# Performance work log

Hardware: AMD Instinct MI355X
Metric: run time of the kernel (lower is better)

The kernel has to match this reference:

```python
import jax, jax.numpy as jnp
import numpy as np

BS, NA, NT, ED, AD, NC = 64, 900, 600, 256, 11, 10
CONF_DECAY = 0.6


def _topk_gather(conf, k, *xs):
    # conf: [bs, N] -> top-k values + gather rows of each x: [bs, N, d] -> [bs, k, d]
    vals, idx = jax.lax.top_k(conf, k)
    outs = [jnp.take_along_axis(x, idx[:, :, None], axis=1) for x in xs]
    return vals, outs


def setup_inputs() -> dict:
    key = jax.random.key(0)
    ks = jax.random.split(key, 7)
    return {
        "instance_feature": jax.random.normal(ks[0], (BS, NA, ED), jnp.float32),
        "anchor": jax.random.normal(ks[1], (BS, NA, AD), jnp.float32),
        "confidence": jax.random.normal(ks[2], (BS, NA, NC), jnp.float32),
        "cached_feature": jax.random.normal(ks[3], (BS, NT, ED), jnp.float32),
        "cached_anchor": jax.random.normal(ks[4], (BS, NT, AD), jnp.float32),
        "prev_confidence": jax.random.uniform(ks[5], (BS, NT), jnp.float32),
        "mask": jax.random.bernoulli(ks[6], 0.8, (BS,)),
    }


def reference(instance_feature, anchor, confidence, cached_feature, cached_anchor, prev_confidence, mask):
    # ---- InstanceBank.update ----
    N = NA - NT  # number of fresh instances kept alongside the temporal cache
    conf_max = confidence.max(axis=-1)  # [bs, NA]
    _, (sel_f, sel_a) = _topk_gather(conf_max, N, instance_feature, anchor)
    sel_f = jnp.concatenate([cached_feature, sel_f], axis=1)  # [bs, NA, ED]
    sel_a = jnp.concatenate([cached_anchor, sel_a], axis=1)   # [bs, NA, AD]
    m = mask[:, None, None]
    feat = jnp.where(m, sel_f, instance_feature)
    anc = jnp.where(m, sel_a, anchor)

    # ---- InstanceBank.cache (detached path) ----
    conf_c = jax.nn.sigmoid(jax.lax.stop_gradient(conf_max))
    conf_c = conf_c.at[:, :NT].set(jnp.maximum(prev_confidence * CONF_DECAY, conf_c[:, :NT]))
    new_conf, (cf, ca) = _topk_gather(
        conf_c, NT, jax.lax.stop_gradient(feat), jax.lax.stop_gradient(anc)
    )

    merged = jnp.concatenate([feat, anc], axis=-1)  # [bs, NA, ED+AD]
    return merged, new_conf, cf, ca
```

## Files before the change

kernel.cpp:

```cpp
#include <hip/hip_runtime.h>

#define BS   64
#define NA   900
#define NT   600
#define NSEL 300
#define ED   256
#define AD   11
#define NC   10
#define SORTN 1024
#define CACHED_FLAG 0x40000000

#define OFF_MERGED  0
#define OFF_NEWCONF (BS * NA * (ED + AD))
#define OFF_CF      (OFF_NEWCONF + BS * NT)
#define OFF_CA      (OFF_CF + BS * NT * ED)

__device__ __forceinline__ unsigned int fkey(float x) {
    unsigned int u = __float_as_uint(x);
    return (u & 0x80000000u) ? ~u : (u | 0x80000000u);
}

__device__ __forceinline__ unsigned long long shfl_xor64(unsigned long long v, int m) {
    return (unsigned long long)__shfl_xor((long long)v, m, 64);
}

__device__ __forceinline__ void sort1024(unsigned long long& key, int i,
                                         unsigned long long* lds) {
    for (int k = 2; k <= SORTN; k <<= 1) {
        for (int j = k >> 1; j > 0; j >>= 1) {
            unsigned long long partner;
            if (j >= 64) {
                __syncthreads();
                lds[i] = key;
                __syncthreads();
                partner = lds[i ^ j];
            } else {
                partner = shfl_xor64(key, j);
            }
            const bool up      = ((i & k) == 0);
            const bool lower   = ((i & j) == 0);
            const bool keepmin = (lower == up);
            const bool pgt     = (key > partner);
            key = (keepmin == pgt) ? partner : key;
        }
    }
}

__global__ __launch_bounds__(1024) void topk_kernel(
    const float* __restrict__ confidence,
    const float* __restrict__ prev_conf,
    const int*   __restrict__ mask,
    float*       __restrict__ new_conf_out,
    int*         __restrict__ src_map,
    int*         __restrict__ pos2)
{
    __shared__ unsigned long long keys[SORTN];
    __shared__ float cc_s[NA];

    const int b = blockIdx.x;
    const int i = threadIdx.x;

    float cmax = 0.0f;
    if (i < NA) {
        const float* cp = confidence + ((size_t)b * NA + i) * NC;
        float m = cp[0];
        #pragma unroll
        for (int k = 1; k < NC; k++) m = fmaxf(m, cp[k]);
        cmax = m;
    }

    unsigned long long key = (i < NA)
        ? ((((unsigned long long)(~fkey(cmax))) << 32) | (unsigned int)i)
        : 0xFFFFFFFFFFFFFFFFull;
    sort1024(key, i, keys);

    __syncthreads();
    int* rank = (int*)keys;
    rank[i] = (int)(key & 0xFFFFFFFFull);
    __syncthreads();

    const int mk = mask[b];
    if (i < NA) {
        int s;
        if (mk) {
            s = (i < NT) ? (i | CACHED_FLAG) : rank[i - NT];
        } else {
            s = i;
        }
        src_map[(size_t)b * NA + i] = s;
    }

    float c = 0.0f;
    if (i < NA) {
        double d = 1.0 / (1.0 + exp(-(double)cmax));
        c = (float)d;
        if (i < NT) c = fmaxf(prev_conf[(size_t)b * NT + i] * 0.6f, c);
        cc_s[i] = c;
    }
    __syncthreads();

    key = (i < NA)
        ? ((((unsigned long long)(~fkey(c))) << 32) | (unsigned int)i)
        : 0xFFFFFFFFFFFFFFFFull;
    sort1024(key, i, keys);

    if (i < NT) {
        int r = (int)(key & 0xFFFFFFFFull);
        new_conf_out[(size_t)b * NT + i] = cc_s[r];
        pos2[(size_t)b * NA + r] = i;
    } else if (i < NA) {
        int r = (int)(key & 0xFFFFFFFFull);
        pos2[(size_t)b * NA + r] = -1;
    }
}

__global__ __launch_bounds__(256) void gather_kernel(
    const float* __restrict__ inst_f,
    const float* __restrict__ anchor,
    const float* __restrict__ cached_f,
    const float* __restrict__ cached_a,
    const int*   __restrict__ src_map,
    const int*   __restrict__ pos2,
    float*       __restrict__ out)
{
    const int wave = threadIdx.x >> 6;
    const int lane = threadIdx.x & 63;
    const int gr   = blockIdx.x * 4 + wave;
    if (gr >= BS * NA) return;

    const int b = gr / NA;
    const int t = gr - b * NA;

    const int s = src_map[(size_t)b * NA + t];
    const int p = pos2[(size_t)b * NA + t];

    const float* fsrc;
    const float* asrc;
    if (s & CACHED_FLAG) {
        const int r = s & 0xFFFF;
        fsrc = cached_f + ((size_t)b * NT + r) * ED;
        asrc = cached_a + ((size_t)b * NT + r) * AD;
    } else {
        fsrc = inst_f + ((size_t)b * NA + s) * ED;
        asrc = anchor + ((size_t)b * NA + s) * AD;
    }

    const float4 v = ((const float4*)fsrc)[lane];
    float av = 0.0f;
    if (lane < AD) av = asrc[lane];

    float* orow = out + OFF_MERGED + ((size_t)b * NA + t) * (ED + AD);
    orow[4 * lane + 0] = v.x;
    orow[4 * lane + 1] = v.y;
    orow[4 * lane + 2] = v.z;
    orow[4 * lane + 3] = v.w;
    if (lane < AD) orow[ED + lane] = av;

    if (p >= 0) {
        float4* crow = (float4*)(out + OFF_CF + ((size_t)b * NT + p) * ED);
        crow[lane] = v;
        if (lane < AD) out[OFF_CA + ((size_t)b * NT + p) * AD + lane] = av;
    }
}

extern "C" void kernel_launch(void* const* d_in, const int* in_sizes, int n_in,
                              void* d_out, int out_size, void* d_ws, size_t ws_size,
                              hipStream_t stream) {
    const float* inst_f = (const float*)d_in[0];
    const float* anchor = (const float*)d_in[1];
    const float* conf   = (const float*)d_in[2];
    const float* cach_f = (const float*)d_in[3];
    const float* cach_a = (const float*)d_in[4];
    const float* prevc  = (const float*)d_in[5];
    const int*   mask   = (const int*)d_in[6];
    float* out = (float*)d_out;

    int* src_map = (int*)d_ws;
    int* pos2    = src_map + BS * NA;

    topk_kernel<<<BS, 1024, 0, stream>>>(conf, prevc, mask,
                                         out + OFF_NEWCONF, src_map, pos2);

    const int nrows = BS * NA;
    gather_kernel<<<(nrows + 3) / 4, 256, 0, stream>>>(
        inst_f, anchor, cach_f, cach_a, src_map, pos2, out);
}
```

Measured before the change: 208.4 us.

## Split the two top-k sorts into separate blocks and use nontemporal gather accesses

The top-k kernel now launches two blocks per batch. One block sorts the raw max-confidence values to build the source map and skips the sort entirely when the mask is off. The other block sorts the sigmoid/decayed confidences for the cache outputs. This doubles block-level parallelism for the serial bitonic sorts, at the cost of computing the per-row confidence max twice. The gather kernel also switches its loads and stores to nontemporal builtins to avoid polluting the cache on the streaming copy.

New measurement: 190.3 us (median of 2 runs). 8.7% less time.

```diff
diff --git a/kernel.cpp b/kernel.cpp
--- a/kernel.cpp
+++ b/kernel.cpp
@@ -14,6 +14,8 @@
 #define OFF_NEWCONF (BS * NA * (ED + AD))
 #define OFF_CF      (OFF_NEWCONF + BS * NT)
 #define OFF_CA      (OFF_CF + BS * NT * ED)
+
+typedef float f32x4 __attribute__((ext_vector_type(4)));
 
 __device__ __forceinline__ unsigned int fkey(float x) {
     unsigned int u = __float_as_uint(x);
@@ -46,6 +48,15 @@
     }
 }
 
+__device__ __forceinline__ float conf_max_row(const float* __restrict__ confidence,
+                                              int b, int i) {
+    const float* cp = confidence + ((size_t)b * NA + i) * NC;
+    float m = cp[0];
+    #pragma unroll
+    for (int k = 1; k < NC; k++) m = fmaxf(m, cp[k]);
+    return m;
+}
+
 __global__ __launch_bounds__(1024) void topk_kernel(
     const float* __restrict__ confidence,
     const float* __restrict__ prev_conf,
@@ -57,60 +68,45 @@
     __shared__ unsigned long long keys[SORTN];
     __shared__ float cc_s[NA];
 
-    const int b = blockIdx.x;
+    const int b = blockIdx.x >> 1;
     const int i = threadIdx.x;
 
-    float cmax = 0.0f;
-    if (i < NA) {
-        const float* cp = confidence + ((size_t)b * NA + i) * NC;
-        float m = cp[0];
-        #pragma unroll
-        for (int k = 1; k < NC; k++) m = fmaxf(m, cp[k]);
-        cmax = m;
-    }
+    if ((blockIdx.x & 1) == 0) {
+        const int mk = mask[b];
+        if (!mk) {
+            if (i < NA) src_map[(size_t)b * NA + i] = i;
+            return;
+        }
+        if (i < NT) src_map[(size_t)b * NA + i] = i | CACHED_FLAG;
 
-    unsigned long long key = (i < NA)
-        ? ((((unsigned long long)(~fkey(cmax))) << 32) | (unsigned int)i)
-        : 0xFFFFFFFFFFFFFFFFull;
-    sort1024(key, i, keys);
-
-    __syncthreads();
-    int* rank = (int*)keys;
-    rank[i] = (int)(key & 0xFFFFFFFFull);
-    __syncthreads();
-
-    const int mk = mask[b];
-    if (i < NA) {
-        int s;
-        if (mk) {
-            s = (i < NT) ? (i | CACHED_FLAG) : rank[i - NT];
-        } else {
-            s = i;
+        float cmax = (i < NA) ? conf_max_row(confidence, b, i) : 0.0f;
+        unsigned long long key = (i < NA)
+            ? ((((unsigned long long)(~fkey(cmax))) << 32) | (unsigned int)i)
+            : 0xFFFFFFFFFFFFFFFFull;
+        sort1024(key, i, keys);
+        if (i < NSEL)
+            src_map[(size_t)b * NA + NT + i] = (int)(key & 0xFFFFFFFFull);
+    } else {
+        float c = 0.0f;
+        if (i < NA) {
+            float cmax = conf_max_row(confidence, b, i);
+            double d = 1.0 / (1.0 + exp(-(double)cmax));
+            c = (float)d;
+            if (i < NT) c = fmaxf(prev_conf[(size_t)b * NT + i] * 0.6f, c);
+            cc_s[i] = c;
         }
-        src_map[(size_t)b * NA + i] = s;
-    }
-
-    float c = 0.0f;
-    if (i < NA) {
-        double d = 1.0 / (1.0 + exp(-(double)cmax));
-        c = (float)d;
-        if (i < NT) c = fmaxf(prev_conf[(size_t)b * NT + i] * 0.6f, c);
-        cc_s[i] = c;
-    }
-    __syncthreads();
-
-    key = (i < NA)
-        ? ((((unsigned long long)(~fkey(c))) << 32) | (unsigned int)i)
-        : 0xFFFFFFFFFFFFFFFFull;
-    sort1024(key, i, keys);
-
-    if (i < NT) {
-        int r = (int)(key & 0xFFFFFFFFull);
-        new_conf_out[(size_t)b * NT + i] = cc_s[r];
-        pos2[(size_t)b * NA + r] = i;
-    } else if (i < NA) {
-        int r = (int)(key & 0xFFFFFFFFull);
-        pos2[(size_t)b * NA + r] = -1;
+        unsigned long long key = (i < NA)
+            ? ((((unsigned long long)(~fkey(c))) << 32) | (unsigned int)i)
+            : 0xFFFFFFFFFFFFFFFFull;
+        sort1024(key, i, keys);
+        if (i < NT) {
+            int r = (int)(key & 0xFFFFFFFFull);
+            new_conf_out[(size_t)b * NT + i] = cc_s[r];
+            pos2[(size_t)b * NA + r] = i;
+        } else if (i < NA) {
+            int r = (int)(key & 0xFFFFFFFFull);
+            pos2[(size_t)b * NA + r] = -1;
+        }
     }
 }
 
@@ -145,21 +141,22 @@
         asrc = anchor + ((size_t)b * NA + s) * AD;
     }
 
-    const float4 v = ((const float4*)fsrc)[lane];
+    const f32x4 v = __builtin_nontemporal_load((const f32x4*)fsrc + lane);
     float av = 0.0f;
     if (lane < AD) av = asrc[lane];
 
     float* orow = out + OFF_MERGED + ((size_t)b * NA + t) * (ED + AD);
-    orow[4 * lane + 0] = v.x;
-    orow[4 * lane + 1] = v.y;
-    orow[4 * lane + 2] = v.z;
-    orow[4 * lane + 3] = v.w;
-    if (lane < AD) orow[ED + lane] = av;
+    __builtin_nontemporal_store(v.x, orow + 4 * lane + 0);
+    __builtin_nontemporal_store(v.y, orow + 4 * lane + 1);
+    __builtin_nontemporal_store(v.z, orow + 4 * lane + 2);
+    __builtin_nontemporal_store(v.w, orow + 4 * lane + 3);
+    if (lane < AD) __builtin_nontemporal_store(av, orow + ED + lane);
 
     if (p >= 0) {
-        float4* crow = (float4*)(out + OFF_CF + ((size_t)b * NT + p) * ED);
-        crow[lane] = v;
-        if (lane < AD) out[OFF_CA + ((size_t)b * NT + p) * AD + lane] = av;
+        f32x4* crow = (f32x4*)(out + OFF_CF + ((size_t)b * NT + p) * ED);
+        __builtin_nontemporal_store(v, crow + lane);
+        if (lane < AD)
+            __builtin_nontemporal_store(av, out + OFF_CA + ((size_t)b * NT + p) * AD + lane);
     }
 }
 
@@ -178,8 +175,8 @@
     int* src_map = (int*)d_ws;
     int* pos2    = src_map + BS * NA;
 
-    topk_kernel<<<BS, 1024, 0, stream>>>(conf, prevc, mask,
-                                         out + OFF_NEWCONF, src_map, pos2);
+    topk_kernel<<<2 * BS, 1024, 0, stream>>>(conf, prevc, mask,
+                                             out + OFF_NEWCONF, src_map, pos2);
 
     const int nrows = BS * NA;
     gather_kernel<<<(nrows + 3) / 4, 256, 0, stream>>>(
```
